# Kernel optimization log

Measured on AMD Instinct MI355X. Metric: run time of the kernel, lower is better.

Reference implementation:

```python
import jax, jax.numpy as jnp
import numpy as np

N = 100000
E = 1600000
NUM_GRAPHS = 64
EPS = 1e-5


def setup_inputs() -> dict:
    key = jax.random.key(0)
    ks = jax.random.split(key, 8)
    x = jax.random.normal(ks[0], (N, 128), dtype=jnp.float32)
    edge_index = jax.random.randint(ks[1], (2, E), 0, N, dtype=jnp.int64)
    batch = jnp.sort(jax.random.randint(ks[2], (N,), 0, NUM_GRAPHS, dtype=jnp.int64))
    W1 = jax.random.normal(ks[3], (128, 128), dtype=jnp.float32) * (1.0 / np.sqrt(128))
    W2 = jax.random.normal(ks[4], (128, 128), dtype=jnp.float32) * (1.0 / np.sqrt(128))
    W3 = jax.random.normal(ks[5], (128, 32), dtype=jnp.float32) * (1.0 / np.sqrt(128))
    return {
        'x': x, 'edge_index': edge_index, 'batch': batch,
        'W1': W1, 'b1': jnp.zeros((128,), jnp.float32),
        'W2': W2, 'b2': jnp.zeros((128,), jnp.float32),
        'W3': W3, 'b3': jnp.zeros((32,), jnp.float32),
        'gamma1': jnp.ones((128,), jnp.float32), 'beta1': jnp.zeros((128,), jnp.float32),
        'gamma2': jnp.ones((128,), jnp.float32), 'beta2': jnp.zeros((128,), jnp.float32),
    }


def _gcn_norm(edge_index, n_nodes):
    # PyG GCNConv default: add self-loops, symmetric normalization.
    loop = jnp.arange(n_nodes, dtype=edge_index.dtype)
    src = jnp.concatenate([edge_index[0], loop])  # [E+N]
    dst = jnp.concatenate([edge_index[1], loop])
    deg = jax.ops.segment_sum(jnp.ones_like(dst, dtype=jnp.float32), dst,
                              num_segments=n_nodes)
    dinv = jnp.where(deg > 0, jax.lax.rsqrt(deg), 0.0)
    norm = dinv[src] * dinv[dst]  # [E+N]
    return src, dst, norm


def _gcn_conv(x, W, b, src, dst, norm, n_nodes):
    h = x @ W                                   # [N, d_out] dense GEMM
    msg = h[src] * norm[:, None]                # gather + scale  [E+N, d_out]
    out = jax.ops.segment_sum(msg, dst, num_segments=n_nodes)  # scatter-add
    return out + b


def _batchnorm(x, gamma, beta):
    # Training-mode BatchNorm1d: batch stats over node dim, biased variance.
    mean = jnp.mean(x, axis=0)
    var = jnp.var(x, axis=0)
    return (x - mean) * jax.lax.rsqrt(var + EPS) * gamma + beta


def reference(x, edge_index, batch, W1, b1, W2, b2, W3, b3,
              gamma1, beta1, gamma2, beta2):
    src, dst, norm = _gcn_norm(edge_index, N)
    h = _gcn_conv(x, W1, b1, src, dst, norm, N)
    h = jax.nn.relu(_batchnorm(h, gamma1, beta1))  # dropout is identity (eval)
    h = _gcn_conv(h, W2, b2, src, dst, norm, N)
    h = jax.nn.relu(_batchnorm(h, gamma2, beta2))
    h = _gcn_conv(h, W3, b3, src, dst, norm, N)
    # global_mean_pool over graph ids
    sums = jax.ops.segment_sum(h, batch, num_segments=NUM_GRAPHS)  # [G, out]
    cnts = jax.ops.segment_sum(jnp.ones((N,), jnp.float32), batch,
                               num_segments=NUM_GRAPHS)
    pooled = sums / jnp.maximum(cnts, 1.0)[:, None]
    return jax.nn.sigmoid(pooled)
```

## Files before the change

kernel.cpp:

```cpp
#include <hip/hip_runtime.h>
#include <math.h>

#define NGRAPH 64
#define EPS_BN 1e-5f
#define BN_BLOCKS 512

typedef unsigned int uint32;
typedef unsigned short ushort16;
typedef __attribute__((ext_vector_type(8))) short short8v;
typedef __attribute__((ext_vector_type(4))) float float4v;

__device__ __forceinline__ float bf2f(uint32 u16) {
    return __uint_as_float(u16 << 16);
}
__device__ __forceinline__ ushort16 f2bf(float f) {
    uint32 u = __float_as_uint(f);
    return (ushort16)((u + 0x7fffu + ((u >> 16) & 1u)) >> 16);
}
__device__ __forceinline__ uint32 pack2(float lo, float hi) {
    return (uint32)f2bf(lo) | ((uint32)f2bf(hi) << 16);
}

#define SC_EPB 8
__global__ __launch_bounds__(256) void k_cnt_w(const int* __restrict__ dst, int* __restrict__ cnt,
                                               int ne, int wsz) {
    const int w = blockIdx.x & 7;
    const int chunk = blockIdx.x >> 3;
    const int wlo = w * wsz;
    const int whi = wlo + wsz;
    int base = chunk * (256 * SC_EPB) + threadIdx.x;
    #pragma unroll
    for (int j = 0; j < SC_EPB; ++j) {
        int i = base + j * 256;
        if (i < ne) {
            int d = dst[i];
            if (d >= wlo && d < whi) atomicAdd(&cnt[d], 1);
        }
    }
}

__global__ __launch_bounds__(1024) void k_scan1(const int* __restrict__ cnt,
                                                int* __restrict__ rowstart,
                                                int* __restrict__ blocksum,
                                                float* __restrict__ dinv, int n) {
    __shared__ int sh[1024];
    const int tid = threadIdx.x;
    const int i = blockIdx.x * 1024 + tid;
    int v = (i < n) ? cnt[i] : 0;
    if (i < n) dinv[i] = rsqrtf((float)(v + 1));
    sh[tid] = v;
    __syncthreads();
    for (int off = 1; off < 1024; off <<= 1) {
        int t = (tid >= off) ? sh[tid - off] : 0;
        __syncthreads();
        sh[tid] += t;
        __syncthreads();
    }
    if (i < n) rowstart[i] = sh[tid] - v;
    if (tid == 1023) blocksum[blockIdx.x] = sh[1023];
}

__global__ __launch_bounds__(1024) void k_scan2(int* __restrict__ blocksum, int nb,
                                                float* __restrict__ psum,
                                                float* __restrict__ pcnt) {
    __shared__ int sh[1024];
    const int tid = threadIdx.x;
    int v = (tid < nb) ? blocksum[tid] : 0;
    sh[tid] = v;
    __syncthreads();
    for (int off = 1; off < 1024; off <<= 1) {
        int t = (tid >= off) ? sh[tid - off] : 0;
        __syncthreads();
        sh[tid] += t;
        __syncthreads();
    }
    if (tid < nb) blocksum[tid] = sh[tid] - v;
    for (int i = tid; i < NGRAPH * 32; i += 1024) psum[i] = 0.f;
    if (tid < NGRAPH) pcnt[tid] = 0.f;
}

__global__ __launch_bounds__(256) void k_scan3(int* __restrict__ rowstart,
                                               int* __restrict__ rowcur,
                                               const int* __restrict__ blocksum, int n) {
    int i = blockIdx.x * 256 + threadIdx.x;
    if (i < n) {
        int v = rowstart[i] + blocksum[i >> 10];
        rowstart[i] = v;
        rowcur[i] = v;
    }
}

__global__ __launch_bounds__(256) void k_scatter_w(const int* __restrict__ src,
                                                   const int* __restrict__ dst,
                                                   int* __restrict__ rowcur,
                                                   int* __restrict__ esrc,
                                                   int ne, int wsz) {
    const int w = blockIdx.x & 7;
    const int chunk = blockIdx.x >> 3;
    const int wlo = w * wsz;
    const int whi = wlo + wsz;
    int base = chunk * (256 * SC_EPB) + threadIdx.x;
    #pragma unroll
    for (int j = 0; j < SC_EPB; ++j) {
        int i = base + j * 256;
        if (i < ne) {
            int d = dst[i];
            if (d >= wlo && d < whi) {
                int pos = atomicAdd(&rowcur[d], 1);
                esrc[pos] = src[i];
            }
        }
    }
}

__global__ __launch_bounds__(256) void k_wprep_all(const float* __restrict__ W1,
                                                   const float* __restrict__ W2,
                                                   const float* __restrict__ W3,
                                                   ushort16* __restrict__ wt1,
                                                   ushort16* __restrict__ wt2,
                                                   ushort16* __restrict__ wt3,
                                                   int* __restrict__ cnt, int n) {
    int i = blockIdx.x * 256 + threadIdx.x;
    if (i < 16384) {
        int c = i >> 7, k = i & 127;
        wt1[i] = f2bf(W1[k * 128 + c]);
    } else if (i < 32768) {
        int j = i - 16384;
        int c = j >> 7, k = j & 127;
        wt2[j] = f2bf(W2[k * 128 + c]);
    } else if (i < 36864) {
        int j = i - 32768;
        int c = j >> 7, k = j & 127;
        wt3[j] = f2bf(W3[k * 32 + c]);
    }
    if (i < n) cnt[i] = 0;
}

template<int COLS, bool BN, bool AF32>
__global__ __launch_bounds__(256) void k_gemm_mfma(const void* __restrict__ Av,
                                                   const ushort16* __restrict__ Wt,
                                                   const float* __restrict__ ss,
                                                   const float* __restrict__ dinv,
                                                   ushort16* __restrict__ C, int nrows) {
    constexpr int K = 128;
    constexpr int LDK = K + 8;
    __shared__ ushort16 As[64 * LDK];
    __shared__ ushort16 Bs[COLS * LDK];
    const int tid = threadIdx.x;

    {
        const uint4* wg = (const uint4*)Wt;
        for (int i = tid; i < COLS * (K / 8); i += 256) {
            int r = i >> 4, c8 = i & 15;
            *(uint4*)&Bs[r * LDK + c8 * 8] = wg[i];
        }
    }

    const int w = tid >> 6;
    const int l = tid & 63;
    const int lr = l & 15;
    const int lg = l >> 4;
    constexpr int CT = COLS / 16;

    #pragma unroll
    for (int half = 0; half < 2; ++half) {
        const int row0 = blockIdx.x * 128 + half * 64;
        if (half) __syncthreads();
        if constexpr (AF32) {
            const float* A = (const float*)Av;
            for (int i = tid; i < 64 * (K / 4); i += 256) {
                int r = i >> 5, c4 = i & 31;
                float4 a;
                if (row0 + r < nrows) a = *(const float4*)&A[(size_t)(row0 + r) * K + c4 * 4];
                else a = make_float4(0.f, 0.f, 0.f, 0.f);
                if (BN) {
                    float4 sc = *(const float4*)&ss[c4 * 4];
                    float4 sh = *(const float4*)&ss[128 + c4 * 4];
                    a.x = fmaxf(fmaf(a.x, sc.x, sh.x), 0.f);
                    a.y = fmaxf(fmaf(a.y, sc.y, sh.y), 0.f);
                    a.z = fmaxf(fmaf(a.z, sc.z, sh.z), 0.f);
                    a.w = fmaxf(fmaf(a.w, sc.w, sh.w), 0.f);
                }
                ushort4 o;
                o.x = f2bf(a.x); o.y = f2bf(a.y); o.z = f2bf(a.z); o.w = f2bf(a.w);
                *(ushort4*)&As[r * LDK + c4 * 4] = o;
            }
        } else {
            const uint4* Ag = (const uint4*)Av;
            for (int i = tid; i < 64 * (K / 8); i += 256) {
                int r = i >> 4, c8 = i & 15;
                uint4 u;
                if (row0 + r < nrows) u = Ag[(size_t)(row0 + r) * 16 + c8];
                else u = make_uint4(0, 0, 0, 0);
                if (BN) {
                    uint32 wv[4] = {u.x, u.y, u.z, u.w};
                    #pragma unroll
                    for (int t = 0; t < 4; ++t) {
                        int f = c8 * 8 + t * 2;
                        float lo = fmaxf(fmaf(bf2f(wv[t] & 0xffffu), ss[f],     ss[128 + f]),     0.f);
                        float hi = fmaxf(fmaf(bf2f(wv[t] >> 16),     ss[f + 1], ss[128 + f + 1]), 0.f);
                        wv[t] = pack2(lo, hi);
                    }
                    u.x = wv[0]; u.y = wv[1]; u.z = wv[2]; u.w = wv[3];
                }
                *(uint4*)&As[r * LDK + c8 * 8] = u;
            }
        }
        __syncthreads();

        float4v acc[CT] = {};
        short8v afrag[4];
        #pragma unroll
        for (int kk = 0; kk < 4; ++kk)
            afrag[kk] = *(const short8v*)&As[(w * 16 + lr) * LDK + kk * 32 + lg * 8];
        #pragma unroll
        for (int kk = 0; kk < 4; ++kk) {
            #pragma unroll
            for (int ct = 0; ct < CT; ++ct) {
                short8v b = *(const short8v*)&Bs[(ct * 16 + lr) * LDK + kk * 32 + lg * 8];
                acc[ct] = __builtin_amdgcn_mfma_f32_16x16x32_bf16(afrag[kk], b, acc[ct], 0, 0, 0);
            }
        }
        #pragma unroll
        for (int r = 0; r < 4; ++r) {
            int gr = row0 + w * 16 + lg * 4 + r;
            if (gr < nrows) {
                float dv = dinv[gr];
                #pragma unroll
                for (int ct = 0; ct < CT; ++ct)
                    C[(size_t)gr * COLS + ct * 16 + lr] = f2bf(acc[ct][r] * dv);
            }
        }
    }
}

template<int COLS>
__global__ __launch_bounds__(256) void k_agg_csr(const ushort16* __restrict__ h,
                                                 const int* __restrict__ rowstart,
                                                 const int* __restrict__ cnt,
                                                 const int* __restrict__ esrc,
                                                 const float* __restrict__ dinv,
                                                 uint32* __restrict__ out, int n) {
    constexpr int TPN = COLS / 2;
    const uint32* __restrict__ hu = (const uint32*)h;
    int gt = blockIdx.x * 256 + threadIdx.x;
    int node = gt / TPN;
    if (node >= n) return;
    int lane = gt % TPN;

    float di = dinv[node];
    uint32 p = hu[(size_t)node * TPN + lane];
    float ax = bf2f(p & 0xffffu);
    float ay = bf2f(p >> 16);

    int beg = rowstart[node];
    int dg = cnt[node];
    if constexpr (TPN == 64) {
        beg = __builtin_amdgcn_readfirstlane(beg);
        dg = __builtin_amdgcn_readfirstlane(dg);
    }
    const int end = beg + dg;
    int e = beg;
    for (; e + 4 <= end; e += 4) {
        int s0 = esrc[e], s1 = esrc[e + 1], s2 = esrc[e + 2], s3 = esrc[e + 3];
        uint32 p0 = hu[(size_t)s0 * TPN + lane];
        uint32 p1 = hu[(size_t)s1 * TPN + lane];
        uint32 p2 = hu[(size_t)s2 * TPN + lane];
        uint32 p3 = hu[(size_t)s3 * TPN + lane];
        ax += bf2f(p0 & 0xffffu); ay += bf2f(p0 >> 16);
        ax += bf2f(p1 & 0xffffu); ay += bf2f(p1 >> 16);
        ax += bf2f(p2 & 0xffffu); ay += bf2f(p2 >> 16);
        ax += bf2f(p3 & 0xffffu); ay += bf2f(p3 >> 16);
    }
    for (; e < end; ++e) {
        int s0 = esrc[e];
        uint32 p0 = hu[(size_t)s0 * TPN + lane];
        ax += bf2f(p0 & 0xffffu);
        ay += bf2f(p0 >> 16);
    }
    out[(size_t)node * TPN + lane] = pack2(ax * di, ay * di);
}

__global__ __launch_bounds__(256) void k_bn_stats1(const uint32* __restrict__ x,
                                                   float* __restrict__ partials, int n) {
    const int cp = threadIdx.x & 63;
    const int rl = threadIdx.x >> 6;
    float s0 = 0.f, s1 = 0.f, q0 = 0.f, q1 = 0.f;
    for (int r = blockIdx.x * 4 + rl; r < n; r += BN_BLOCKS * 4) {
        uint32 u = x[(size_t)r * 64 + cp];
        float lo = bf2f(u & 0xffffu), hi = bf2f(u >> 16);
        s0 += lo; s1 += hi;
        q0 = fmaf(lo, lo, q0); q1 = fmaf(hi, hi, q1);
    }
    __shared__ float shs[4 * 128];
    __shared__ float shq[4 * 128];
    shs[rl * 128 + 2 * cp] = s0; shs[rl * 128 + 2 * cp + 1] = s1;
    shq[rl * 128 + 2 * cp] = q0; shq[rl * 128 + 2 * cp + 1] = q1;
    __syncthreads();
    int f = threadIdx.x;
    if (f < 128) {
        float s = shs[f] + shs[128 + f] + shs[256 + f] + shs[384 + f];
        float q = shq[f] + shq[128 + f] + shq[256 + f] + shq[384 + f];
        partials[(size_t)blockIdx.x * 256 + f] = s;
        partials[(size_t)blockIdx.x * 256 + 128 + f] = q;
    }
}

__global__ __launch_bounds__(256) void k_bn_stats2(const float* __restrict__ partials,
                                                   const float* __restrict__ gamma,
                                                   const float* __restrict__ beta,
                                                   float* __restrict__ ss, int n) {
    const int f16 = threadIdx.x & 15;
    const int rl = threadIdx.x >> 4;
    const int f = blockIdx.x * 16 + f16;
    float s = 0.f, q = 0.f;
    for (int r = rl; r < BN_BLOCKS; r += 16) {
        s += partials[(size_t)r * 256 + f];
        q += partials[(size_t)r * 256 + 128 + f];
    }
    __shared__ float shs[256], shq[256];
    shs[threadIdx.x] = s;
    shq[threadIdx.x] = q;
    __syncthreads();
    if (rl == 0) {
        float S = 0.f, Q = 0.f;
        #pragma unroll
        for (int r = 0; r < 16; ++r) { S += shs[r * 16 + f16]; Q += shq[r * 16 + f16]; }
        float inv_n = 1.0f / (float)n;
        float mean = S * inv_n;
        float var = Q * inv_n - mean * mean;
        float scale = gamma[f] * rsqrtf(var + EPS_BN);
        ss[f] = scale;
        ss[128 + f] = beta[f] - mean * scale;
    }
}

#define POOL_SLICE 128
__global__ __launch_bounds__(256) void k_pool2(const uint32* __restrict__ h3,
                                               const int* __restrict__ batch,
                                               float* __restrict__ sums,
                                               float* __restrict__ cnt, int n) {
    const int fp = threadIdx.x & 15;
    const int sub = threadIdx.x >> 4;
    int node0 = blockIdx.x * (16 * POOL_SLICE) + sub * POOL_SLICE;
    if (node0 >= n) return;
    int node1 = min(node0 + POOL_SLICE, n);

    int cur_g = batch[node0];
    float a0 = 0.f, a1 = 0.f, c = 0.f;
    for (int i = node0; i < node1; ++i) {
        int g = batch[i];
        if (g != cur_g) {
            atomicAdd(&sums[cur_g * 32 + 2 * fp], a0);
            atomicAdd(&sums[cur_g * 32 + 2 * fp + 1], a1);
            if (fp == 0) atomicAdd(&cnt[cur_g], c);
            a0 = 0.f; a1 = 0.f; c = 0.f; cur_g = g;
        }
        uint32 u = h3[(size_t)i * 16 + fp];
        a0 += bf2f(u & 0xffffu);
        a1 += bf2f(u >> 16);
        c += 1.f;
    }
    atomicAdd(&sums[cur_g * 32 + 2 * fp], a0);
    atomicAdd(&sums[cur_g * 32 + 2 * fp + 1], a1);
    if (fp == 0) atomicAdd(&cnt[cur_g], c);
}

__global__ __launch_bounds__(256) void k_final(const float* __restrict__ sums,
                                               const float* __restrict__ cnt,
                                               const float* __restrict__ b3,
                                               float* __restrict__ out) {
    int i = blockIdx.x * 256 + threadIdx.x;
    if (i >= NGRAPH * 32) return;
    int g = i >> 5;
    int f = i & 31;
    float c = fmaxf(cnt[g], 1.0f);
    float v = sums[i] / c + b3[f];
    out[i] = 1.0f / (1.0f + expf(-v));
}

extern "C" void kernel_launch(void* const* d_in, const int* in_sizes, int n_in,
                              void* d_out, int out_size, void* d_ws, size_t ws_size,
                              hipStream_t stream) {
    const float* x      = (const float*)d_in[0];
    const int*   eidx   = (const int*)d_in[1];
    const int*   batch  = (const int*)d_in[2];
    const float* W1     = (const float*)d_in[3];
    const float* W2     = (const float*)d_in[5];
    const float* W3     = (const float*)d_in[7];
    const float* b3     = (const float*)d_in[8];
    const float* gamma1 = (const float*)d_in[9];
    const float* beta1  = (const float*)d_in[10];
    const float* gamma2 = (const float*)d_in[11];
    const float* beta2  = (const float*)d_in[12];

    const int N = in_sizes[0] / 128;
    const int E = in_sizes[1] / 2;
    const int* src = eidx;
    const int* dst = eidx + E;

    size_t off = 0;
    auto carve = [&](size_t bytes) {
        char* p = (char*)d_ws + off;
        off += (bytes + 511) & ~(size_t)511;
        return p;
    };
    const size_t NB = (size_t)N * 128 * sizeof(float);
    ushort16* bufA  = (ushort16*)carve(NB / 2);
    uint32* bufB    = (uint32*)carve(NB / 2);
    int*   cnt      = (int*)carve((size_t)N * 4);
    int*   rowstart = (int*)carve((size_t)N * 4);
    int*   rowcur   = (int*)carve((size_t)N * 4);
    float* dinv     = (float*)carve((size_t)N * 4);
    int*   esrc     = (int*)carve((size_t)E * 4);
    ushort16* wt1   = (ushort16*)carve(128 * 128 * 2);
    ushort16* wt2   = (ushort16*)carve(128 * 128 * 2);
    ushort16* wt3   = (ushort16*)carve(32 * 128 * 2);
    float* ss1      = (float*)carve(256 * 4);
    float* ss2      = (float*)carve(256 * 4);
    float* partials = (float*)carve((size_t)BN_BLOCKS * 256 * 4);
    int*   blocksum = (int*)carve(1024 * 4);
    float* psum     = (float*)carve(NGRAPH * 32 * 4);
    float* pcnt     = (float*)carve(NGRAPH * 4);
    (void)ws_size; (void)n_in; (void)out_size;

    const int nblkN   = (N + 255) / 256;
    const int nbScan  = (N + 1023) / 1024;
    const int nbGemm  = (N + 127) / 128;
    const int nblkAgg128 = ((size_t)N * 64 + 255) / 256;
    const int nblkAgg32  = ((size_t)N * 16 + 255) / 256;
    const int nblkPool   = (N + 16 * POOL_SLICE - 1) / (16 * POOL_SLICE);
    const int wsz        = (N + 7) / 8;
    const int nbScat     = ((E + 256 * SC_EPB - 1) / (256 * SC_EPB)) * 8;
    const int nbWprep    = (((36864 > N) ? 36864 : N) + 255) / 256;

    k_wprep_all<<<nbWprep, 256, 0, stream>>>(W1, W2, W3, wt1, wt2, wt3, cnt, N);

    k_cnt_w<<<nbScat, 256, 0, stream>>>(dst, cnt, E, wsz);
    k_scan1<<<nbScan, 1024, 0, stream>>>(cnt, rowstart, blocksum, dinv, N);
    k_scan2<<<1, 1024, 0, stream>>>(blocksum, nbScan, psum, pcnt);
    k_scan3<<<nblkN, 256, 0, stream>>>(rowstart, rowcur, blocksum, N);
    k_scatter_w<<<nbScat, 256, 0, stream>>>(src, dst, rowcur, esrc, E, wsz);

    k_gemm_mfma<128, false, true><<<nbGemm, 256, 0, stream>>>(x, wt1, nullptr, dinv, bufA, N);
    k_agg_csr<128><<<nblkAgg128, 256, 0, stream>>>(bufA, rowstart, cnt, esrc, dinv, bufB, N);
    k_bn_stats1<<<BN_BLOCKS, 256, 0, stream>>>(bufB, partials, N);
    k_bn_stats2<<<8, 256, 0, stream>>>(partials, gamma1, beta1, ss1, N);

    k_gemm_mfma<128, true, false><<<nbGemm, 256, 0, stream>>>(bufB, wt2, ss1, dinv, bufA, N);
    k_agg_csr<128><<<nblkAgg128, 256, 0, stream>>>(bufA, rowstart, cnt, esrc, dinv, bufB, N);
    k_bn_stats1<<<BN_BLOCKS, 256, 0, stream>>>(bufB, partials, N);
    k_bn_stats2<<<8, 256, 0, stream>>>(partials, gamma2, beta2, ss2, N);

    k_gemm_mfma<32, true, false><<<nbGemm, 256, 0, stream>>>(bufB, wt3, ss2, dinv, bufA, N);
    k_agg_csr<32><<<nblkAgg32, 256, 0, stream>>>(bufA, rowstart, cnt, esrc, dinv, bufB, N);

    k_pool2<<<nblkPool, 256, 0, stream>>>(bufB, batch, psum, pcnt, N);
    k_final<<<(NGRAPH * 32 + 255) / 256, 256, 0, stream>>>(psum, pcnt, b3, (float*)d_out);
}
```

Before: 459.9 us.

## Build CSR with per-edge rank from count atomics, drop windowed scatter atomics

```diff
diff --git a/kernel.cpp b/kernel.cpp
--- a/kernel.cpp
+++ b/kernel.cpp
@@ -21,22 +21,11 @@
     return (uint32)f2bf(lo) | ((uint32)f2bf(hi) << 16);
 }
 
-#define SC_EPB 8
-__global__ __launch_bounds__(256) void k_cnt_w(const int* __restrict__ dst, int* __restrict__ cnt,
-                                               int ne, int wsz) {
-    const int w = blockIdx.x & 7;
-    const int chunk = blockIdx.x >> 3;
-    const int wlo = w * wsz;
-    const int whi = wlo + wsz;
-    int base = chunk * (256 * SC_EPB) + threadIdx.x;
-    #pragma unroll
-    for (int j = 0; j < SC_EPB; ++j) {
-        int i = base + j * 256;
-        if (i < ne) {
-            int d = dst[i];
-            if (d >= wlo && d < whi) atomicAdd(&cnt[d], 1);
-        }
-    }
+__global__ __launch_bounds__(256) void k_cnt_r(const int* __restrict__ dst,
+                                               int* __restrict__ cnt,
+                                               int* __restrict__ rank, int ne) {
+    int i = blockIdx.x * 256 + threadIdx.x;
+    if (i < ne) rank[i] = atomicAdd(&cnt[dst[i]], 1);
 }
 
 __global__ __launch_bounds__(1024) void k_scan1(const int* __restrict__ cnt,
@@ -80,37 +69,18 @@
 }
 
 __global__ __launch_bounds__(256) void k_scan3(int* __restrict__ rowstart,
-                                               int* __restrict__ rowcur,
                                                const int* __restrict__ blocksum, int n) {
     int i = blockIdx.x * 256 + threadIdx.x;
-    if (i < n) {
-        int v = rowstart[i] + blocksum[i >> 10];
-        rowstart[i] = v;
-        rowcur[i] = v;
-    }
-}
-
-__global__ __launch_bounds__(256) void k_scatter_w(const int* __restrict__ src,
-                                                   const int* __restrict__ dst,
-                                                   int* __restrict__ rowcur,
-                                                   int* __restrict__ esrc,
-                                                   int ne, int wsz) {
-    const int w = blockIdx.x & 7;
-    const int chunk = blockIdx.x >> 3;
-    const int wlo = w * wsz;
-    const int whi = wlo + wsz;
-    int base = chunk * (256 * SC_EPB) + threadIdx.x;
-    #pragma unroll
-    for (int j = 0; j < SC_EPB; ++j) {
-        int i = base + j * 256;
-        if (i < ne) {
-            int d = dst[i];
-            if (d >= wlo && d < whi) {
-                int pos = atomicAdd(&rowcur[d], 1);
-                esrc[pos] = src[i];
-            }
-        }
-    }
+    if (i < n) rowstart[i] += blocksum[i >> 10];
+}
+
+__global__ __launch_bounds__(256) void k_scatter_nr(const int* __restrict__ src,
+                                                    const int* __restrict__ dst,
+                                                    const int* __restrict__ rank,
+                                                    const int* __restrict__ rowstart,
+                                                    int* __restrict__ esrc, int ne) {
+    int i = blockIdx.x * 256 + threadIdx.x;
+    if (i < ne) esrc[rowstart[dst[i]] + rank[i]] = src[i];
 }
 
 __global__ __launch_bounds__(256) void k_wprep_all(const float* __restrict__ W1,
@@ -410,9 +380,9 @@
     uint32* bufB    = (uint32*)carve(NB / 2);
     int*   cnt      = (int*)carve((size_t)N * 4);
     int*   rowstart = (int*)carve((size_t)N * 4);
-    int*   rowcur   = (int*)carve((size_t)N * 4);
     float* dinv     = (float*)carve((size_t)N * 4);
     int*   esrc     = (int*)carve((size_t)E * 4);
+    int*   rank     = (int*)carve((size_t)E * 4);
     ushort16* wt1   = (ushort16*)carve(128 * 128 * 2);
     ushort16* wt2   = (ushort16*)carve(128 * 128 * 2);
     ushort16* wt3   = (ushort16*)carve(32 * 128 * 2);
@@ -425,22 +395,21 @@
     (void)ws_size; (void)n_in; (void)out_size;
 
     const int nblkN   = (N + 255) / 256;
+    const int nblkE   = (E + 255) / 256;
     const int nbScan  = (N + 1023) / 1024;
     const int nbGemm  = (N + 127) / 128;
     const int nblkAgg128 = ((size_t)N * 64 + 255) / 256;
     const int nblkAgg32  = ((size_t)N * 16 + 255) / 256;
     const int nblkPool   = (N + 16 * POOL_SLICE - 1) / (16 * POOL_SLICE);
-    const int wsz        = (N + 7) / 8;
-    const int nbScat     = ((E + 256 * SC_EPB - 1) / (256 * SC_EPB)) * 8;
     const int nbWprep    = (((36864 > N) ? 36864 : N) + 255) / 256;
 
     k_wprep_all<<<nbWprep, 256, 0, stream>>>(W1, W2, W3, wt1, wt2, wt3, cnt, N);
 
-    k_cnt_w<<<nbScat, 256, 0, stream>>>(dst, cnt, E, wsz);
+    k_cnt_r<<<nblkE, 256, 0, stream>>>(dst, cnt, rank, E);
     k_scan1<<<nbScan, 1024, 0, stream>>>(cnt, rowstart, blocksum, dinv, N);
     k_scan2<<<1, 1024, 0, stream>>>(blocksum, nbScan, psum, pcnt);
-    k_scan3<<<nblkN, 256, 0, stream>>>(rowstart, rowcur, blocksum, N);
-    k_scatter_w<<<nbScat, 256, 0, stream>>>(src, dst, rowcur, esrc, E, wsz);
+    k_scan3<<<nblkN, 256, 0, stream>>>(rowstart, blocksum, N);
+    k_scatter_nr<<<nblkE, 256, 0, stream>>>(src, dst, rank, rowstart, esrc, E);
 
     k_gemm_mfma<128, false, true><<<nbGemm, 256, 0, stream>>>(x, wt1, nullptr, dinv, bufA, N);
     k_agg_csr<128><<<nblkAgg128, 256, 0, stream>>>(bufA, rowstart, cnt, esrc, dinv, bufB, N);
```

Result: faster. 411.3 us (-10.6%).
